# Performance work log

Measured on AMD Instinct MI355X. Metric: run time of the kernel, lower is better.

Reference implementation:

```python
import jax, jax.numpy as jnp
import numpy as np

B, N, D, E = 256, 192, 512, 1024
H = E // 2          # MLP hidden = 512
K = 58              # round(0.3 * 192), hardcoded in the torch forward
EPS_L2 = 1e-8
EPS_BN = 1e-5


def setup_inputs() -> dict:
    key = jax.random.key(0)
    ks = jax.random.split(key, 8)
    s = 0.02
    return {
        "all_patch_embeddings": jax.random.normal(ks[0], (B, N, D), dtype=jnp.float32),
        "attention_map": jax.random.uniform(ks[1], (B, N + 1, N + 1), dtype=jnp.float32),
        # fc: Linear(D, E)
        "W_fc": jax.random.normal(ks[2], (E, D), dtype=jnp.float32) * s,
        "b_fc": jnp.zeros((E,), dtype=jnp.float32),
        # mlp layer 0: Linear(D, H) + BatchNorm1d(H) + ReLU
        "W1": jax.random.normal(ks[3], (H, D), dtype=jnp.float32) * s,
        "b1": jnp.zeros((H,), dtype=jnp.float32),
        "gamma1": jnp.ones((H,), dtype=jnp.float32),
        "beta1": jnp.zeros((H,), dtype=jnp.float32),
        # mlp layer 1: Linear(H, E) (no BN/ReLU applied on last layer)
        "W2": jax.random.normal(ks[4], (E, H), dtype=jnp.float32) * s,
        "b2": jnp.zeros((E,), dtype=jnp.float32),
    }


def reference(all_patch_embeddings, attention_map, W_fc, b_fc, W1, b1, gamma1, beta1, W2, b2):
    # CLS-row attention over the 192 patch tokens: [B, N]
    cls_attn = attention_map[:, 0, 1:]
    # torch.sort(descending)[...,:K] == top-k indices (batched, replaces python loop)
    _, idx = jax.lax.top_k(cls_attn, K)                      # [B, K] int32
    # batched gather replacing the per-sample index_select loop
    sel = jnp.take_along_axis(all_patch_embeddings, idx[:, :, None], axis=1)  # [B, K, D]
    # l2norm over last dim
    norm = jnp.sqrt(jnp.sum(sel * sel, axis=-1, keepdims=True)) + EPS_L2
    base = sel / norm
    # .half() cast in the original (round-trip to fp16 precision)
    base = base.astype(jnp.float16).astype(jnp.float32)
    # fc branch
    feat_fc = jnp.einsum('bkd,ed->bke', base, W_fc) + b_fc    # [B, K, E]
    # mlp branch (num_layers=2): Linear -> BN(train-mode batch stats) -> ReLU -> Linear
    h = jnp.einsum('bkd,hd->bkh', base, W1) + b1              # [B, K, H]
    hf = h.reshape(B * K, H)
    mu = jnp.mean(hf, axis=0)
    var = jnp.var(hf, axis=0)
    hf = (hf - mu) * jax.lax.rsqrt(var + EPS_BN) * gamma1 + beta1
    h = jax.nn.relu(hf).reshape(B, K, H)
    feat_mlp = jnp.einsum('bkh,eh->bke', h, W2) + b2          # [B, K, E]
    feats = feat_mlp + feat_fc
    # maxk_pool1d_var with k=1 and lengths == K reduces to max over token dim
    return jnp.max(feats, axis=1).astype(jnp.float32)         # [B, E]
```

## Files before the change

### kernel.cpp

```cpp
#include <hip/hip_runtime.h>
#include <hip/hip_fp16.h>

#define B_ 256
#define N_ 192
#define D_ 512
#define E_ 1024
#define H_ 512
#define K_ 58
#define M_ (B_*K_)
#define M2_ (B_*64)

typedef _Float16 f16;
typedef unsigned int u32;
typedef _Float16 half8 __attribute__((ext_vector_type(8)));
typedef float floatx16 __attribute__((ext_vector_type(16)));

__device__ inline half8 cvt8(float4 f0, float4 f1) {
  half8 r;
  r[0]=(f16)f0.x; r[1]=(f16)f0.y; r[2]=(f16)f0.z; r[3]=(f16)f0.w;
  r[4]=(f16)f1.x; r[5]=(f16)f1.y; r[6]=(f16)f1.z; r[7]=(f16)f1.w;
  return r;
}

__device__ inline void gl_lds16(const f16* g, f16* l) {
  __builtin_amdgcn_global_load_lds((const __attribute__((address_space(1))) u32*)g,
                                   (__attribute__((address_space(3))) u32*)l, 16, 0, 0);
}

__device__ inline void stage128(const f16* gbase, int gstride, f16* sT, int w, int lane) {
  int lrow  = lane >> 2;
  int chunk = (lane & 3) ^ ((lane >> 3) & 3);
  gl_lds16(gbase + (size_t)(w*16      + lrow)*gstride + chunk*8, &sT[(w*16)*32]);
  gl_lds16(gbase + (size_t)(64 + w*16 + lrow)*gstride + chunk*8, &sT[(64 + w*16)*32]);
}

__global__ void setup_kernel(const float* __restrict__ Wfc, const float* __restrict__ W2,
                             const float* __restrict__ W1, const float* __restrict__ attn,
                             const float* __restrict__ emb,
                             f16* __restrict__ Wcat, f16* __restrict__ W1_16,
                             f16* __restrict__ A16, float* __restrict__ csum) {
  __shared__ float sv[N_];
  __shared__ int sidx[K_];
  __shared__ int cnt;
  int blk = blockIdx.x, t = threadIdx.x;
  if (blk < 512) {
    int idx = (blk*256 + t)*8;
    int e = idx >> 10, c = idx & 1023;
    const float* src = (c < 512) ? (Wfc + (size_t)e*512 + c)
                                 : (W2  + (size_t)e*512 + (c-512));
    half8 o = cvt8(((const float4*)src)[0], ((const float4*)src)[1]);
    *(uint4*)(Wcat + idx) = *(uint4*)&o;
  } else if (blk < 640) {
    int idx = ((blk-512)*256 + t)*8;
    const float* src = W1 + idx;
    half8 o = cvt8(((const float4*)src)[0], ((const float4*)src)[1]);
    *(uint4*)(W1_16 + idx) = *(uint4*)&o;
  } else if (blk < 896) {
    int b = blk - 640;
    if (t == 0) cnt = 0;
    if (t < N_) sv[t] = attn[(size_t)b*193*193 + 1 + t];
    __syncthreads();
    if (t < N_) {
      float v = sv[t]; int rank = 0;
      for (int j = 0; j < N_; ++j) {
        float vj = sv[j];
        rank += (vj > v) || (vj == v && j < t);
      }
      if (rank < K_) sidx[atomicAdd(&cnt, 1)] = t;
    }
    __syncthreads();
    int w = t >> 6, lane = t & 63;
    for (int slot = w; slot < 64; slot += 4) {
      f16* dst = A16 + ((size_t)b*64 + slot)*1024 + lane*8;
      if (slot < K_) {
        const float* src = emb + ((size_t)b*N_ + sidx[slot])*D_ + lane*8;
        float4 v0 = ((const float4*)src)[0];
        float4 v1 = ((const float4*)src)[1];
        float s = v0.x*v0.x + v0.y*v0.y + v0.z*v0.z + v0.w*v0.w
                + v1.x*v1.x + v1.y*v1.y + v1.z*v1.z + v1.w*v1.w;
        #pragma unroll
        for (int off = 32; off > 0; off >>= 1) s += __shfl_xor(s, off);
        float inv = 1.0f / (sqrtf(s) + 1e-8f);
        half8 o;
        o[0]=(f16)(v0.x*inv); o[1]=(f16)(v0.y*inv); o[2]=(f16)(v0.z*inv); o[3]=(f16)(v0.w*inv);
        o[4]=(f16)(v1.x*inv); o[5]=(f16)(v1.y*inv); o[6]=(f16)(v1.z*inv); o[7]=(f16)(v1.w*inv);
        *(uint4*)dst = *(uint4*)&o;
      } else {
        uint4 z; z.x=0u; z.y=0u; z.z=0u; z.w=0u;
        *(uint4*)dst = z;
      }
    }
  } else {
    float4 z; z.x=0.f; z.y=0.f; z.z=0.f; z.w=0.f;
    ((float4*)csum)[t] = z;
  }
}

__launch_bounds__(256, 2)
__global__ void gemm1_kernel(const f16* __restrict__ A16, const f16* __restrict__ W1_16,
                             const float* __restrict__ b1, f16* __restrict__ Aout,
                             float* __restrict__ csum, float* __restrict__ css) {
  __shared__ f16 sA[2][128*32];
  __shared__ f16 sB[2][128*32];
  __shared__ float sSum[4][64], sSS[4][64];
  int t = threadIdx.x;
  int g = blockIdx.x;
  int xcd = g & 7, rest = g >> 3;
  int n0 = (rest & 3) * 128;
  int m0 = (xcd + 8*(rest >> 2)) * 128;
  int lane = t & 63, w = t >> 6;
  int l31 = lane & 31, khalf = lane >> 5, swz = (l31 >> 1) & 3;
  int rw = w & 1, cw = w >> 1;
  floatx16 acc[2][2] = {};
  const f16* Ab = A16 + (size_t)m0*1024;
  const f16* Bb = W1_16 + (size_t)n0*512;
  stage128(Ab, 1024, sA[0], w, lane);
  stage128(Bb, 512,  sB[0], w, lane);
  __syncthreads();
  for (int it = 0; it < 16; ++it) {
    int cur = it & 1, nxt = cur ^ 1;
    if (it < 15) {
      stage128(Ab + (it+1)*32, 1024, sA[nxt], w, lane);
      stage128(Bb + (it+1)*32, 512,  sB[nxt], w, lane);
    }
    #pragma unroll
    for (int s = 0; s < 2; ++s) {
      int ko = ((s*2 + khalf) ^ swz) * 8;
      half8 a[2], bf[2];
      #pragma unroll
      for (int i = 0; i < 2; ++i) a[i]  = *(const half8*)&sA[cur][(rw*64 + i*32 + l31)*32 + ko];
      #pragma unroll
      for (int j = 0; j < 2; ++j) bf[j] = *(const half8*)&sB[cur][(cw*64 + j*32 + l31)*32 + ko];
      #pragma unroll
      for (int i = 0; i < 2; ++i)
        #pragma unroll
        for (int j = 0; j < 2; ++j)
          acc[i][j] = __builtin_amdgcn_mfma_f32_32x32x16_f16(a[i], bf[j], acc[i][j], 0, 0, 0);
    }
    __syncthreads();
  }
  #pragma unroll
  for (int jt = 0; jt < 2; ++jt) {
    int col = n0 + cw*64 + jt*32 + l31;
    float bias = b1[col];
    float s = 0.f, ss = 0.f;
    #pragma unroll
    for (int i = 0; i < 2; ++i) {
      #pragma unroll
      for (int rg = 0; rg < 16; ++rg) {
        int rib = i*32 + (rg&3) + 8*(rg>>2) + 4*khalf;
        float x = acc[i][jt][rg] + bias;
        Aout[(size_t)(m0 + rw*64 + rib)*1024 + 512 + col] = (f16)x;
        if (i == 0 || rib < K_) { s += x; ss += x*x; }
      }
    }
    s  += __shfl_xor(s, 32);
    ss += __shfl_xor(ss, 32);
    if (lane < 32) { sSum[w][jt*32 + l31] = s; sSS[w][jt*32 + l31] = ss; }
  }
  __syncthreads();
  if (t < 128) {
    int c = t;
    int w0 = 2*(c >> 6), ci = c & 63;
    atomicAdd(&csum[n0 + c], sSum[w0][ci] + sSum[w0+1][ci]);
    atomicAdd(&css[n0 + c],  sSS[w0][ci]  + sSS[w0+1][ci]);
  }
}

__global__ void bnrelu_kernel(f16* __restrict__ A, const float* __restrict__ csum,
                              const float* __restrict__ css, const float* __restrict__ gamma,
                              const float* __restrict__ beta) {
  int t = threadIdx.x, lane = t & 63, w = t >> 6;
  int col = lane * 8;
  float sc[8], sh[8];
  #pragma unroll
  for (int j = 0; j < 8; ++j) {
    int c = col + j;
    float mu  = csum[c] * (1.0f/M_);
    float var = css[c] * (1.0f/M_) - mu*mu;
    float s   = gamma[c] * rsqrtf(var + 1e-5f);
    sc[j] = s; sh[j] = beta[c] - mu*s;
  }
  int r0 = blockIdx.x * 16 + w;
  #pragma unroll
  for (int i = 0; i < 4; ++i) {
    f16* p = A + (size_t)(r0 + i*4)*1024 + 512 + col;
    uint4 u = *(const uint4*)p;
    half8 v = *(half8*)&u, o;
    #pragma unroll
    for (int j = 0; j < 8; ++j) o[j] = (f16)fmaxf((float)v[j]*sc[j] + sh[j], 0.f);
    *(uint4*)p = *(uint4*)&o;
  }
}

__launch_bounds__(256, 3)
__global__ void fused_kernel(const f16* __restrict__ A16, const f16* __restrict__ Wcat,
                             const float* __restrict__ bfc, const float* __restrict__ b2,
                             float* __restrict__ out) {
  __shared__ f16 sA[2][128*32];
  __shared__ f16 sB[2][128*32];
  __shared__ float sMax[4][64];
  int t = threadIdx.x;
  int g = blockIdx.x;
  int xcd = g & 7, rest = g >> 3;
  int e0 = (rest & 7) * 128;
  int bm = xcd + 8*(rest >> 3);
  int lane = t & 63, w = t >> 6;
  int l31 = lane & 31, khalf = lane >> 5, swz = (l31 >> 1) & 3;
  int rw = w & 1, cw = w >> 1;
  floatx16 acc[2][2] = {};
  const f16* Ab = A16 + (size_t)bm*128*1024;
  const f16* Bb = Wcat + (size_t)e0*1024;
  stage128(Ab, 1024, sA[0], w, lane);
  stage128(Bb, 1024, sB[0], w, lane);
  __syncthreads();
  for (int it = 0; it < 32; ++it) {
    int cur = it & 1, nxt = cur ^ 1;
    if (it < 31) {
      stage128(Ab + (it+1)*32, 1024, sA[nxt], w, lane);
      stage128(Bb + (it+1)*32, 1024, sB[nxt], w, lane);
    }
    #pragma unroll
    for (int s = 0; s < 2; ++s) {
      int ko = ((s*2 + khalf) ^ swz) * 8;
      half8 a[2], bf[2];
      #pragma unroll
      for (int i = 0; i < 2; ++i) a[i]  = *(const half8*)&sA[cur][(rw*64 + i*32 + l31)*32 + ko];
      #pragma unroll
      for (int j = 0; j < 2; ++j) bf[j] = *(const half8*)&sB[cur][(cw*64 + j*32 + l31)*32 + ko];
      #pragma unroll
      for (int i = 0; i < 2; ++i)
        #pragma unroll
        for (int j = 0; j < 2; ++j)
          acc[i][j] = __builtin_amdgcn_mfma_f32_32x32x16_f16(a[i], bf[j], acc[i][j], 0, 0, 0);
    }
    __syncthreads();
  }
  #pragma unroll
  for (int jt = 0; jt < 2; ++jt) {
    float mx = -3.0e38f;
    #pragma unroll
    for (int i = 0; i < 2; ++i) {
      #pragma unroll
      for (int rg = 0; rg < 16; ++rg) {
        int rib = i*32 + (rg&3) + 8*(rg>>2) + 4*khalf;
        if (i == 0 || rib < K_) mx = fmaxf(mx, acc[i][jt][rg]);
      }
    }
    mx = fmaxf(mx, __shfl_xor(mx, 32));
    if (lane < 32) sMax[w][jt*32 + l31] = mx;
  }
  __syncthreads();
  #pragma unroll
  for (int bb = 0; bb < 2; ++bb) {
    int c = t & 127;
    if ((t >> 7) == bb) {
      float mx = sMax[bb + 2*(c >> 6)][c & 63];
      int e = e0 + c;
      out[((size_t)bm*2 + bb)*E_ + e] = mx + bfc[e] + b2[e];
    }
  }
}

extern "C" void kernel_launch(void* const* d_in, const int* in_sizes, int n_in,
                              void* d_out, int out_size, void* d_ws, size_t ws_size,
                              hipStream_t stream) {
  const float* emb   = (const float*)d_in[0];
  const float* attn  = (const float*)d_in[1];
  const float* Wfc   = (const float*)d_in[2];
  const float* bfc   = (const float*)d_in[3];
  const float* W1    = (const float*)d_in[4];
  const float* b1    = (const float*)d_in[5];
  const float* gamma = (const float*)d_in[6];
  const float* beta  = (const float*)d_in[7];
  const float* W2    = (const float*)d_in[8];
  const float* b2    = (const float*)d_in[9];
  float* out = (float*)d_out;

  char* ws = (char*)d_ws;
  f16*   A16   = (f16*)(ws);
  f16*   Wcat  = (f16*)(ws + 33554432);
  f16*   W1_16 = (f16*)(ws + 35651584);
  float* csum  = (float*)(ws + 36175872);
  float* css   = (float*)(ws + 36177920);

  setup_kernel<<<897, 256, 0, stream>>>(Wfc, W2, W1, attn, emb, Wcat, W1_16, A16, csum);
  gemm1_kernel<<<512, 256, 0, stream>>>(A16, W1_16, b1, A16, csum, css);
  bnrelu_kernel<<<1024, 256, 0, stream>>>(A16, csum, css, gamma, beta);
  fused_kernel<<<1024, 256, 0, stream>>>(A16, Wcat, bfc, b2, out);
}
```

Baseline: 241.9 us.

## Enlarge fused GEMM tile to 256x256 with ping-pong staged MFMA schedule

```diff
diff --git a/kernel.cpp b/kernel.cpp
--- a/kernel.cpp
+++ b/kernel.cpp
@@ -15,6 +15,11 @@
 typedef _Float16 half8 __attribute__((ext_vector_type(8)));
 typedef float floatx16 __attribute__((ext_vector_type(16)));
 
+#define WAIT_VMCNT0() asm volatile("s_waitcnt vmcnt(0)" ::: "memory")
+#define BAR()         __builtin_amdgcn_s_barrier()
+#define PRIO1()       __builtin_amdgcn_s_setprio(1)
+#define PRIO0()       __builtin_amdgcn_s_setprio(0)
+
 __device__ inline half8 cvt8(float4 f0, float4 f1) {
   half8 r;
   r[0]=(f16)f0.x; r[1]=(f16)f0.y; r[2]=(f16)f0.z; r[3]=(f16)f0.w;
@@ -32,6 +37,14 @@
   int chunk = (lane & 3) ^ ((lane >> 3) & 3);
   gl_lds16(gbase + (size_t)(w*16      + lrow)*gstride + chunk*8, &sT[(w*16)*32]);
   gl_lds16(gbase + (size_t)(64 + w*16 + lrow)*gstride + chunk*8, &sT[(64 + w*16)*32]);
+}
+
+__device__ inline void stage_half(const f16* gbase, f16* sT, int h, int w, int lane) {
+  int lrow = lane >> 3;
+  int cg   = (lane & 7) ^ lrow;
+  int r0 = h*128 + w*16;
+  gl_lds16(gbase + (size_t)(r0     + lrow)*1024 + cg*8, &sT[(size_t)r0*64]);
+  gl_lds16(gbase + (size_t)(r0 + 8 + lrow)*1024 + cg*8, &sT[(size_t)(r0 + 8)*64]);
 }
 
 __global__ void setup_kernel(const float* __restrict__ Wfc, const float* __restrict__ W2,
@@ -193,72 +206,123 @@
   }
 }
 
-__launch_bounds__(256, 3)
+__launch_bounds__(512, 2)
 __global__ void fused_kernel(const f16* __restrict__ A16, const f16* __restrict__ Wcat,
                              const float* __restrict__ bfc, const float* __restrict__ b2,
                              float* __restrict__ out) {
-  __shared__ f16 sA[2][128*32];
-  __shared__ f16 sB[2][128*32];
-  __shared__ float sMax[4][64];
+  __shared__ __align__(16) f16 sA[2][256*64];
+  __shared__ __align__(16) f16 sB[2][256*64];
+  __shared__ float sMax[4][256];
   int t = threadIdx.x;
   int g = blockIdx.x;
   int xcd = g & 7, rest = g >> 3;
-  int e0 = (rest & 7) * 128;
-  int bm = xcd + 8*(rest >> 3);
+  int nt = rest & 3;
+  int bt = xcd + 8*(rest >> 2);
+  int e0 = nt * 256;
   int lane = t & 63, w = t >> 6;
-  int l31 = lane & 31, khalf = lane >> 5, swz = (l31 >> 1) & 3;
-  int rw = w & 1, cw = w >> 1;
-  floatx16 acc[2][2] = {};
-  const f16* Ab = A16 + (size_t)bm*128*1024;
+  int l31 = lane & 31, khalf = lane >> 5, swzr = l31 & 7;
+  int wm = w >> 2, wn = w & 3;
+  floatx16 acc[4][2] = {};
+  const f16* Ab = A16 + (size_t)bt*256*1024;
   const f16* Bb = Wcat + (size_t)e0*1024;
-  stage128(Ab, 1024, sA[0], w, lane);
-  stage128(Bb, 1024, sB[0], w, lane);
+  int aBase0 = (wm*128 +  0 + l31)*64;
+  int aBase1 = (wm*128 + 32 + l31)*64;
+  int aBase2 = (wm*128 + 64 + l31)*64;
+  int aBase3 = (wm*128 + 96 + l31)*64;
+  int bBase0 = (wn*64  +  0 + l31)*64;
+  int bBase1 = (wn*64  + 32 + l31)*64;
+  stage_half(Ab, sA[0], 0, w, lane);
+  stage_half(Ab, sA[0], 1, w, lane);
+  stage_half(Bb, sB[0], 0, w, lane);
+  stage_half(Bb, sB[0], 1, w, lane);
+  WAIT_VMCNT0(); BAR();
+  int cur = 0;
+  #pragma unroll 1
+  for (int it = 0; it < 16; ++it) {
+    int nxt = cur ^ 1;
+    const f16* An = Ab + (it+1)*64;
+    const f16* Bn = Bb + (it+1)*64;
+    const f16* sAc = sA[cur];
+    const f16* sBc = sB[cur];
+    half8 a0f[4], a1f[4], a2f[4], a3f[4], b0v[4], b1v[4];
+    #pragma unroll
+    for (int s = 0; s < 4; ++s) {
+      int ko = (((s<<1)|khalf) ^ swzr) << 3;
+      a0f[s] = *(const half8*)&sAc[aBase0 + ko];
+      a1f[s] = *(const half8*)&sAc[aBase1 + ko];
+      b0v[s] = *(const half8*)&sBc[bBase0 + ko];
+    }
+    if (it < 15) stage_half(An, sA[nxt], 0, w, lane);
+    BAR(); PRIO1();
+    #pragma unroll
+    for (int s = 0; s < 4; ++s) {
+      acc[0][0] = __builtin_amdgcn_mfma_f32_32x32x16_f16(a0f[s], b0v[s], acc[0][0], 0,0,0);
+      acc[1][0] = __builtin_amdgcn_mfma_f32_32x32x16_f16(a1f[s], b0v[s], acc[1][0], 0,0,0);
+    }
+    PRIO0(); BAR();
+    #pragma unroll
+    for (int s = 0; s < 4; ++s) {
+      int ko = (((s<<1)|khalf) ^ swzr) << 3;
+      b1v[s] = *(const half8*)&sBc[bBase1 + ko];
+    }
+    if (it < 15) stage_half(An, sA[nxt], 1, w, lane);
+    BAR(); PRIO1();
+    #pragma unroll
+    for (int s = 0; s < 4; ++s) {
+      acc[0][1] = __builtin_amdgcn_mfma_f32_32x32x16_f16(a0f[s], b1v[s], acc[0][1], 0,0,0);
+      acc[1][1] = __builtin_amdgcn_mfma_f32_32x32x16_f16(a1f[s], b1v[s], acc[1][1], 0,0,0);
+    }
+    PRIO0(); BAR();
+    #pragma unroll
+    for (int s = 0; s < 4; ++s) {
+      int ko = (((s<<1)|khalf) ^ swzr) << 3;
+      a2f[s] = *(const half8*)&sAc[aBase2 + ko];
+      a3f[s] = *(const half8*)&sAc[aBase3 + ko];
+    }
+    if (it < 15) stage_half(Bn, sB[nxt], 0, w, lane);
+    BAR(); PRIO1();
+    #pragma unroll
+    for (int s = 0; s < 4; ++s) {
+      acc[2][1] = __builtin_amdgcn_mfma_f32_32x32x16_f16(a2f[s], b1v[s], acc[2][1], 0,0,0);
+      acc[3][1] = __builtin_amdgcn_mfma_f32_32x32x16_f16(a3f[s], b1v[s], acc[3][1], 0,0,0);
+    }
+    PRIO0(); BAR();
+    if (it < 15) stage_half(Bn, sB[nxt], 1, w, lane);
+    BAR(); PRIO1();
+    #pragma unroll
+    for (int s = 0; s < 4; ++s) {
+      acc[2][0] = __builtin_amdgcn_mfma_f32_32x32x16_f16(a2f[s], b0v[s], acc[2][0], 0,0,0);
+      acc[3][0] = __builtin_amdgcn_mfma_f32_32x32x16_f16(a3f[s], b0v[s], acc[3][0], 0,0,0);
+    }
+    PRIO0();
+    WAIT_VMCNT0();
+    BAR();
+    cur = nxt;
+  }
+  #pragma unroll
+  for (int p = 0; p < 2; ++p) {
+    #pragma unroll
+    for (int nf = 0; nf < 2; ++nf) {
+      float mx = -3.0e38f;
+      #pragma unroll
+      for (int rg = 0; rg < 16; ++rg)
+        mx = fmaxf(mx, acc[2*p][nf][rg]);
+      #pragma unroll
+      for (int rg = 0; rg < 16; ++rg) {
+        int rowin = (rg&3) + 8*(rg>>2) + 4*khalf;
+        if (rowin < K_ - 32) mx = fmaxf(mx, acc[2*p+1][nf][rg]);
+      }
+      mx = fmaxf(mx, __shfl_xor(mx, 32));
+      if (lane < 32) sMax[wm*2 + p][wn*64 + nf*32 + l31] = mx;
+    }
+  }
   __syncthreads();
-  for (int it = 0; it < 32; ++it) {
-    int cur = it & 1, nxt = cur ^ 1;
-    if (it < 31) {
-      stage128(Ab + (it+1)*32, 1024, sA[nxt], w, lane);
-      stage128(Bb + (it+1)*32, 1024, sB[nxt], w, lane);
-    }
-    #pragma unroll
-    for (int s = 0; s < 2; ++s) {
-      int ko = ((s*2 + khalf) ^ swz) * 8;
-      half8 a[2], bf[2];
-      #pragma unroll
-      for (int i = 0; i < 2; ++i) a[i]  = *(const half8*)&sA[cur][(rw*64 + i*32 + l31)*32 + ko];
-      #pragma unroll
-      for (int j = 0; j < 2; ++j) bf[j] = *(const half8*)&sB[cur][(cw*64 + j*32 + l31)*32 + ko];
-      #pragma unroll
-      for (int i = 0; i < 2; ++i)
-        #pragma unroll
-        for (int j = 0; j < 2; ++j)
-          acc[i][j] = __builtin_amdgcn_mfma_f32_32x32x16_f16(a[i], bf[j], acc[i][j], 0, 0, 0);
-    }
-    __syncthreads();
-  }
-  #pragma unroll
-  for (int jt = 0; jt < 2; ++jt) {
-    float mx = -3.0e38f;
-    #pragma unroll
-    for (int i = 0; i < 2; ++i) {
-      #pragma unroll
-      for (int rg = 0; rg < 16; ++rg) {
-        int rib = i*32 + (rg&3) + 8*(rg>>2) + 4*khalf;
-        if (i == 0 || rib < K_) mx = fmaxf(mx, acc[i][jt][rg]);
-      }
-    }
-    mx = fmaxf(mx, __shfl_xor(mx, 32));
-    if (lane < 32) sMax[w][jt*32 + l31] = mx;
-  }
-  __syncthreads();
-  #pragma unroll
-  for (int bb = 0; bb < 2; ++bb) {
-    int c = t & 127;
-    if ((t >> 7) == bb) {
-      float mx = sMax[bb + 2*(c >> 6)][c & 63];
-      int e = e0 + c;
-      out[((size_t)bm*2 + bb)*E_ + e] = mx + bfc[e] + b2[e];
-    }
+  #pragma unroll
+  for (int j = 0; j < 2; ++j) {
+    int idx = t + j*512;
+    int bq = idx >> 8, c = idx & 255;
+    int e = e0 + c;
+    out[((size_t)bt*4 + bq)*E_ + e] = sMax[bq][c] + bfc[e] + b2[e];
   }
 }
 
@@ -287,5 +351,5 @@
   setup_kernel<<<897, 256, 0, stream>>>(Wfc, W2, W1, attn, emb, Wcat, W1_16, A16, csum);
   gemm1_kernel<<<512, 256, 0, stream>>>(A16, W1_16, b1, A16, csum, css);
   bnrelu_kernel<<<1024, 256, 0, stream>>>(A16, csum, css, gamma, beta);
-  fused_kernel<<<1024, 256, 0, stream>>>(A16, Wcat, bfc, b2, out);
-}
+  fused_kernel<<<256, 512, 0, stream>>>(A16, Wcat, bfc, b2, out);
+}
```

After: 236.6 us. -2.2%, faster.
